# Performance work log

Hardware: AMD Instinct MI355X
Metric: run time of the kernel (lower is better)

The kernel has to match this reference:

```python
import jax, jax.numpy as jnp
import numpy as np

B, L, N, HS, HD, C = 4, 200, 160, 768, 256, 16  # batch, bert len, word len, bert hidden, dense hidden, classes


def setup_inputs() -> dict:
    key = jax.random.key(0)
    ks = jax.random.split(key, 8)
    transformer_out = jax.random.normal(ks[0], (B, L + 1, HS), dtype=jnp.float32)
    word_mapback = jnp.sort(jax.random.randint(ks[1], (B, L), 0, N), axis=-1)
    token_length = jnp.maximum(jax.random.randint(ks[2], (B,), 0, N), N // 2)
    length = jnp.maximum(jax.random.randint(ks[3], (B,), 0, L), 3 * L // 4)
    Wd = jax.random.normal(ks[4], (HS, HD), dtype=jnp.float32) * 0.02
    bd = jnp.zeros((HD,), dtype=jnp.float32)
    Wc = jax.random.normal(ks[5], (3 * HD, C), dtype=jnp.float32) * 0.02
    bc = jnp.zeros((C,), dtype=jnp.float32)
    return dict(transformer_out=transformer_out, Wd=Wd, bd=bd, Wc=Wc, bc=bc,
                word_mapback=word_mapback, token_length=token_length, length=length)


def reference(transformer_out, Wd, bd, Wc, bc, word_mapback, token_length, length):
    # mask over bert positions (after dropping CLS at index 0)
    bert_indi = (jnp.arange(L) < length[:, None]).astype(jnp.float32)[..., None]   # [B,L,1]
    h = transformer_out[:, 1:L + 1, :] * bert_indi                                  # [B,L,HS]
    onehot = jax.nn.one_hot(word_mapback, N, dtype=jnp.float32) * bert_indi         # [B,L,N]
    dense_h = h @ Wd + bd                                                           # [B,L,HD]
    # word-piece -> word mean pooling (one-hot bmm + count normalize)
    pooled = jnp.einsum('bln,blh->bnh', onehot, dense_h)                             # [B,N,HD]
    wnt = onehot.sum(axis=1)                                                         # [B,N]
    pooled = pooled / jnp.where(wnt == 0, 1.0, wnt)[..., None]
    # candidate (i,j) upper-triangular valid-span mask
    tok_mask = (jnp.arange(N) < token_length[:, None]).astype(jnp.float32)           # [B,N]
    cand = jnp.triu(jnp.ones((N, N), jnp.float32))[None] * (tok_mask[:, None, :] * tok_mask[:, :, None])  # [B,N,N]
    # boundary features: [start_repr ; end_repr]
    boundary = jnp.concatenate([
        jnp.broadcast_to(pooled[:, :, None, :], (B, N, N, HD)),
        jnp.broadcast_to(pooled[:, None, :, :], (B, N, N, HD))], axis=-1) * cand[..., None]
    # span sums: span[b,i,k,d] = sum_{i<=j<=k} pooled[b,j,d]*tok_mask[b,j], via prefix sums
    pv = jnp.cumsum(pooled * tok_mask[..., None], axis=1)                            # P[k]
    pv0 = jnp.concatenate([jnp.zeros((B, 1, HD), pv.dtype), pv[:, :-1]], axis=1)     # P[i-1]
    span = (pv[:, None, :, :] - pv0[:, :, None, :]) * cand[..., None]                # [B,N,N,HD]
    # span averaging: divide by span length (k - i + 1), clamped to 1 elsewhere
    diff = jnp.arange(1, N + 1)[None, :] - jnp.arange(N)[:, None]                    # diff[i,k] = k+1-i
    span = span / jnp.where(diff > 0, diff, 1).astype(jnp.float32)[None, :, :, None]
    table = jnp.concatenate([boundary, span], axis=-1)                               # [B,N,N,3*HD]
    logits = (table @ Wc + bc) * cand[..., None]                                     # [B,N,N,C]
    return logits
```

## Files before the change

kernel.cpp:

```cpp
#include <hip/hip_runtime.h>

#define B 4
#define L 200
#define N 160
#define HS 768
#define HD 256
#define C 16

#define KP 784
#define WJ 48
#define NROW (B * N)
#define WCT_STRIDE 260
#define KH 40

typedef float f4v __attribute__((ext_vector_type(4)));

__global__ __launch_bounds__(256) void wfull_kernel(
    const float* __restrict__ Wd,
    const float* __restrict__ bd,
    const float* __restrict__ Wc,
    float* __restrict__ Wfull)
{
    const int blk = blockIdx.x;
    const int t = threadIdx.x;

    if (blk < 144) {
        const int kb = blk / 3;
        const int m  = blk % 3;

        __shared__ float wcT[16 * WCT_STRIDE];
        for (int e = t; e < HD * C; e += 256) {
            const int d = e >> 4, c = e & 15;
            wcT[c * WCT_STRIDE + d] = Wc[(size_t)(m * HD + d) * C + c];
        }
        __syncthreads();

        const int kl = t >> 4, c = t & 15;
        const int k = kb * 16 + kl;
        const float4* wd4 = (const float4*)(Wd + (size_t)k * HD);
        const float4* wc4 = (const float4*)(wcT + c * WCT_STRIDE);
        float acc = 0.f;
        #pragma unroll 8
        for (int q = 0; q < HD / 4; ++q) {
            const float4 a = wd4[q];
            const float4 w = wc4[q];
            acc += a.x * w.x + a.y * w.y + a.z * w.z + a.w * w.w;
        }
        Wfull[(size_t)k * WJ + m * 16 + c] = acc;
    } else {
        if (t < WJ) {
            const int m = t >> 4, c = t & 15;
            float acc = 0.f;
            #pragma unroll 8
            for (int q = 0; q < HD / 4; ++q) {
                const int d = 4 * q;
                const float4 w = *(const float4*)(bd + d);
                acc += w.x * Wc[(size_t)(m * HD + d) * C + c]
                     + w.y * Wc[(size_t)(m * HD + d + 1) * C + c]
                     + w.z * Wc[(size_t)(m * HD + d + 2) * C + c]
                     + w.w * Wc[(size_t)(m * HD + d + 3) * C + c];
            }
            Wfull[(size_t)768 * WJ + t] = acc;
        }
        for (int e = t; e < WJ * 15; e += 256) {
            const int k = 769 + e / WJ, j = e % WJ;
            Wfull[(size_t)k * WJ + j] = 0.f;
        }
    }
}

__global__ __launch_bounds__(256) void poolgemm_kernel(
    const float* __restrict__ TO,
    const float* __restrict__ Wfull,
    const int*   __restrict__ wm,
    const int*   __restrict__ lengths,
    const int*   __restrict__ token_length,
    float* __restrict__ AB,
    float* __restrict__ Tg)
{
    const int row = blockIdx.x;
    const int t   = threadIdx.x;
    const int b   = row / N, n = row % N;

    __shared__ int   smap[L];
    __shared__ float hsL[KP];
    __shared__ float pLDS[4 * WJ];

    for (int e = t; e < L; e += 256) smap[e] = wm[b * L + e];
    __syncthreads();

    const int len = lengths[b];
    int lo = 0, hi = L;
    while (lo < hi) { int m = (lo + hi) >> 1; if (smap[m] < n) lo = m + 1; else hi = m; }
    int lo2 = lo, hi2 = L;
    while (lo2 < hi2) { int m = (lo2 + hi2) >> 1; if (smap[m] < n + 1) lo2 = m + 1; else hi2 = m; }
    const int start = lo < len ? lo : len;
    const int stop  = lo2 < len ? lo2 : len;
    const float ci  = (stop > start) ? 1.0f / (float)(stop - start) : 0.0f;

    if (t < 192) {
        float4 a = {0.f, 0.f, 0.f, 0.f};
        const float* base = TO + ((size_t)b * (L + 1) + 1) * HS + 4 * t;
        for (int l = start; l < stop; ++l) {
            const float4 r = *(const float4*)(base + (size_t)l * HS);
            a.x += r.x; a.y += r.y; a.z += r.z; a.w += r.w;
        }
        a.x *= ci; a.y *= ci; a.z *= ci; a.w *= ci;
        *(float4*)&hsL[4 * t] = a;
    } else if (t < 208) {
        hsL[768 + (t - 192)] = (t == 192 && stop > start) ? 1.0f : 0.0f;
    }
    __syncthreads();

    if (t < 192) {
        const int j  = t % WJ;
        const int ks = t / WJ;
        const int k0 = ks * 196;
        const float* wf = Wfull + j;
        float acc = 0.f;
        #pragma unroll 7
        for (int q = 0; q < 49; ++q) {
            const int k = k0 + 4 * q;
            const float4 h = *(const float4*)&hsL[k];
            acc += h.x * wf[(size_t)k * WJ]       + h.y * wf[(size_t)(k + 1) * WJ]
                 + h.z * wf[(size_t)(k + 2) * WJ] + h.w * wf[(size_t)(k + 3) * WJ];
        }
        pLDS[ks * WJ + j] = acc;
    }
    __syncthreads();

    if (t < WJ) {
        const float v = pLDS[t] + pLDS[WJ + t] + pLDS[2 * WJ + t] + pLDS[3 * WJ + t];
        if (t < 32) AB[(size_t)row * 32 + t] = v;
        else        Tg[(size_t)row * 16 + (t - 32)] = (n < token_length[b]) ? v : 0.f;
    }
}

__global__ __launch_bounds__(256) void finalize_kernel(
    const float* __restrict__ AB,
    const float* __restrict__ T,
    const float* __restrict__ bc,
    const int*   __restrict__ token_length,
    f4v* __restrict__ out)
{
    const int it = blockIdx.x;
    const int kh = blockIdx.y;
    const int b  = blockIdx.z;
    const int t  = threadIdx.x;
    const int tl = token_length[b];

    __shared__ float sT[N * 16];
    __shared__ float sB[KH * 16];
    __shared__ float sA[8 * 16];
    __shared__ float sS[(N + 1) * 16];
    __shared__ float pref[16 * 16];

    {
        const float4* T4 = (const float4*)(T + (size_t)b * N * 16);
        float4* sT4 = (float4*)sT;
        for (int e = t; e < N * 4; e += 256) sT4[e] = T4[e];
    }
    if (t < KH * 4) {
        const int kl = t >> 2, cq = t & 3;
        *(float4*)&sB[kl * 16 + cq * 4] =
            *(const float4*)&AB[((size_t)b * N + kh * KH + kl) * 32 + 16 + cq * 4];
    }
    if (t >= 192 && t < 224) {
        const int il = (t - 192) >> 2, cq = t & 3;
        *(float4*)&sA[il * 16 + cq * 4] =
            *(const float4*)&AB[((size_t)b * N + it * 8 + il) * 32 + cq * 4];
    }
    if (t >= 224 && t < 240) sS[t - 224] = 0.f;
    __syncthreads();

    const int c = t & 15, g = t >> 4;
    const int nb = g * 10;
    {
        float run = 0.f;
        for (int u = 0; u < 10; ++u) {
            run += sT[(nb + u) * 16 + c];
            sS[(nb + u + 1) * 16 + c] = run;
        }
        pref[g * 16 + c] = run;
    }
    __syncthreads();
    if (t < 16) {
        float off = 0.f;
        for (int g2 = 0; g2 < 16; ++g2) {
            const float tmp = pref[g2 * 16 + t];
            pref[g2 * 16 + t] = off;
            off += tmp;
        }
    }
    __syncthreads();
    {
        const float off = pref[g * 16 + c];
        for (int u = 0; u < 10; ++u) sS[(nb + u + 1) * 16 + c] += off;
    }
    __syncthreads();

    for (int q = 0; q < 5; ++q) {
        const int qid = t + q * 256;
        const int cq  = qid & 3;
        const int kl  = (qid >> 2) % KH;
        const int il  = (qid >> 2) / KH;
        const int i   = it * 8 + il;
        const int k   = kh * KH + kl;

        f4v v = {0.f, 0.f, 0.f, 0.f};
        if ((i <= k) & (i < tl) & (k < tl)) {
            const float4 a   = *(const float4*)&sA[il * 16 + cq * 4];
            const float4 bb  = *(const float4*)&sB[kl * 16 + cq * 4];
            const float4 sk  = *(const float4*)&sS[(k + 1) * 16 + cq * 4];
            const float4 si  = *(const float4*)&sS[i * 16 + cq * 4];
            const float4 bcq = *(const float4*)&bc[cq * 4];
            const float inv = 1.0f / (float)(k - i + 1);
            v.x = a.x + bb.x + (sk.x - si.x) * inv + bcq.x;
            v.y = a.y + bb.y + (sk.y - si.y) * inv + bcq.y;
            v.z = a.z + bb.z + (sk.z - si.z) * inv + bcq.z;
            v.w = a.w + bb.w + (sk.w - si.w) * inv + bcq.w;
        }
        __builtin_nontemporal_store(v, &out[((size_t)(b * N + i) * N + k) * 4 + cq]);
    }
}

extern "C" void kernel_launch(void* const* d_in, const int* in_sizes, int n_in,
                              void* d_out, int out_size, void* d_ws, size_t ws_size,
                              hipStream_t stream) {
    const float* TO    = (const float*)d_in[0];
    const float* Wd    = (const float*)d_in[1];
    const float* bd    = (const float*)d_in[2];
    const float* Wc    = (const float*)d_in[3];
    const float* bc    = (const float*)d_in[4];
    const int*   wm    = (const int*)d_in[5];
    const int*   tokl  = (const int*)d_in[6];
    const int*   lenp  = (const int*)d_in[7];

    float* ws    = (float*)d_ws;
    float* Wfull = ws;
    float* AB    = Wfull + (size_t)KP * WJ;
    float* Tg    = AB + (size_t)NROW * 32;

    wfull_kernel<<<145, 256, 0, stream>>>(Wd, bd, Wc, Wfull);
    poolgemm_kernel<<<NROW, 256, 0, stream>>>(TO, Wfull, wm, lenp, tokl, AB, Tg);
    finalize_kernel<<<dim3(20, 4, B), 256, 0, stream>>>(AB, Tg, bc, tokl, (f4v*)d_out);
}
```

Before: 29.52 us.

## Precompute word intervals in weight kernel and prefetch Wfull slice in poolgemm

The per-word binary search over word_mapback moves out of poolgemm into four extra blocks of the weight-fusion kernel, which write packed start/stop intervals to workspace. Poolgemm then drops the shared-map load and its barrier and shrinks to 192 threads. Each thread also preloads its first 32 Wfull values into registers before the pooling sum, so the global loads overlap the TO accumulation. The cost is higher register pressure and one more small workspace array.

Result: slower. 31.03 us (+5.1%).

```diff
diff --git a/kernel.cpp b/kernel.cpp
--- a/kernel.cpp
+++ b/kernel.cpp
@@ -19,7 +19,10 @@
     const float* __restrict__ Wd,
     const float* __restrict__ bd,
     const float* __restrict__ Wc,
-    float* __restrict__ Wfull)
+    const int*   __restrict__ wm,
+    const int*   __restrict__ lengths,
+    float* __restrict__ Wfull,
+    int*   __restrict__ ivl)
 {
     const int blk = blockIdx.x;
     const int t = threadIdx.x;
@@ -47,7 +50,7 @@
             acc += a.x * w.x + a.y * w.y + a.z * w.z + a.w * w.w;
         }
         Wfull[(size_t)k * WJ + m * 16 + c] = acc;
-    } else {
+    } else if (blk == 144) {
         if (t < WJ) {
             const int m = t >> 4, c = t & 15;
             float acc = 0.f;
@@ -66,14 +69,29 @@
             const int k = 769 + e / WJ, j = e % WJ;
             Wfull[(size_t)k * WJ + j] = 0.f;
         }
-    }
-}
-
-__global__ __launch_bounds__(256) void poolgemm_kernel(
+    } else {
+        const int b = blk - 145;
+        __shared__ int smap[L];
+        for (int e = t; e < L; e += 256) smap[e] = wm[b * L + e];
+        __syncthreads();
+        if (t < N) {
+            const int n = t;
+            const int len = lengths[b];
+            int lo = 0, hi = L;
+            while (lo < hi) { int m = (lo + hi) >> 1; if (smap[m] < n) lo = m + 1; else hi = m; }
+            int lo2 = lo, hi2 = L;
+            while (lo2 < hi2) { int m = (lo2 + hi2) >> 1; if (smap[m] < n + 1) lo2 = m + 1; else hi2 = m; }
+            const int start = lo < len ? lo : len;
+            const int stop  = lo2 < len ? lo2 : len;
+            ivl[b * N + n] = start | (stop << 16);
+        }
+    }
+}
+
+__global__ __launch_bounds__(192) void poolgemm_kernel(
     const float* __restrict__ TO,
     const float* __restrict__ Wfull,
-    const int*   __restrict__ wm,
-    const int*   __restrict__ lengths,
+    const int*   __restrict__ ivl,
     const int*   __restrict__ token_length,
     float* __restrict__ AB,
     float* __restrict__ Tg)
@@ -82,23 +100,22 @@
     const int t   = threadIdx.x;
     const int b   = row / N, n = row % N;
 
-    __shared__ int   smap[L];
     __shared__ float hsL[KP];
     __shared__ float pLDS[4 * WJ];
 
-    for (int e = t; e < L; e += 256) smap[e] = wm[b * L + e];
-    __syncthreads();
-
-    const int len = lengths[b];
-    int lo = 0, hi = L;
-    while (lo < hi) { int m = (lo + hi) >> 1; if (smap[m] < n) lo = m + 1; else hi = m; }
-    int lo2 = lo, hi2 = L;
-    while (lo2 < hi2) { int m = (lo2 + hi2) >> 1; if (smap[m] < n + 1) lo2 = m + 1; else hi2 = m; }
-    const int start = lo < len ? lo : len;
-    const int stop  = lo2 < len ? lo2 : len;
-    const float ci  = (stop > start) ? 1.0f / (float)(stop - start) : 0.0f;
-
-    if (t < 192) {
+    const int j  = t % WJ;
+    const int ks = t / WJ;
+    const int k0 = ks * 196;
+    const float* wf = Wfull + j;
+    float pre[32];
+    #pragma unroll
+    for (int kk = 0; kk < 32; ++kk) pre[kk] = wf[(size_t)(k0 + kk) * WJ];
+
+    const int v = ivl[row];
+    const int start = v & 0xFFFF, stop = v >> 16;
+    const float ci = (stop > start) ? 1.0f / (float)(stop - start) : 0.0f;
+
+    {
         float4 a = {0.f, 0.f, 0.f, 0.f};
         const float* base = TO + ((size_t)b * (L + 1) + 1) * HS + 4 * t;
         for (int l = start; l < stop; ++l) {
@@ -107,32 +124,31 @@
         }
         a.x *= ci; a.y *= ci; a.z *= ci; a.w *= ci;
         *(float4*)&hsL[4 * t] = a;
-    } else if (t < 208) {
-        hsL[768 + (t - 192)] = (t == 192 && stop > start) ? 1.0f : 0.0f;
-    }
-    __syncthreads();
-
-    if (t < 192) {
-        const int j  = t % WJ;
-        const int ks = t / WJ;
-        const int k0 = ks * 196;
-        const float* wf = Wfull + j;
-        float acc = 0.f;
-        #pragma unroll 7
-        for (int q = 0; q < 49; ++q) {
-            const int k = k0 + 4 * q;
-            const float4 h = *(const float4*)&hsL[k];
-            acc += h.x * wf[(size_t)k * WJ]       + h.y * wf[(size_t)(k + 1) * WJ]
-                 + h.z * wf[(size_t)(k + 2) * WJ] + h.w * wf[(size_t)(k + 3) * WJ];
-        }
-        pLDS[ks * WJ + j] = acc;
-    }
+        if (t < 16) hsL[768 + t] = (t == 0 && stop > start) ? 1.0f : 0.0f;
+    }
+    __syncthreads();
+
+    float acc = 0.f;
+    #pragma unroll
+    for (int q = 0; q < 8; ++q) {
+        const float4 h = *(const float4*)&hsL[k0 + 4 * q];
+        acc += h.x * pre[4 * q]     + h.y * pre[4 * q + 1]
+             + h.z * pre[4 * q + 2] + h.w * pre[4 * q + 3];
+    }
+    #pragma unroll 5
+    for (int q = 8; q < 49; ++q) {
+        const int k = k0 + 4 * q;
+        const float4 h = *(const float4*)&hsL[k];
+        acc += h.x * wf[(size_t)k * WJ]       + h.y * wf[(size_t)(k + 1) * WJ]
+             + h.z * wf[(size_t)(k + 2) * WJ] + h.w * wf[(size_t)(k + 3) * WJ];
+    }
+    pLDS[ks * WJ + j] = acc;
     __syncthreads();
 
     if (t < WJ) {
-        const float v = pLDS[t] + pLDS[WJ + t] + pLDS[2 * WJ + t] + pLDS[3 * WJ + t];
-        if (t < 32) AB[(size_t)row * 32 + t] = v;
-        else        Tg[(size_t)row * 16 + (t - 32)] = (n < token_length[b]) ? v : 0.f;
+        const float vv = pLDS[t] + pLDS[WJ + t] + pLDS[2 * WJ + t] + pLDS[3 * WJ + t];
+        if (t < 32) AB[(size_t)row * 32 + t] = vv;
+        else        Tg[(size_t)row * 16 + (t - 32)] = (n < token_length[b]) ? vv : 0.f;
     }
 }
 
@@ -240,8 +256,9 @@
     float* Wfull = ws;
     float* AB    = Wfull + (size_t)KP * WJ;
     float* Tg    = AB + (size_t)NROW * 32;
-
-    wfull_kernel<<<145, 256, 0, stream>>>(Wd, bd, Wc, Wfull);
-    poolgemm_kernel<<<NROW, 256, 0, stream>>>(TO, Wfull, wm, lenp, tokl, AB, Tg);
+    int*   ivl   = (int*)(Tg + (size_t)NROW * 16);
+
+    wfull_kernel<<<149, 256, 0, stream>>>(Wd, bd, Wc, wm, lenp, Wfull, ivl);
+    poolgemm_kernel<<<NROW, 192, 0, stream>>>(TO, Wfull, ivl, tokl, AB, Tg);
     finalize_kernel<<<dim3(20, 4, B), 256, 0, stream>>>(AB, Tg, bc, tokl, (f4v*)d_out);
 }
```
